# Optimization experiments

Measured on AMD Instinct MI355X. Metric: run time of the kernel, lower is better.

The kernel has to match this reference:

```python
import jax, jax.numpy as jnp
import numpy as np

K = 4          # deform conv kernel size
STRIDE = 4     # deform conv stride (no padding)
EPS = 1e-5     # BatchNorm eps
SLOPE = 0.01   # LeakyReLU default negative slope


def conv2d(x, w, b, stride):
    out = jax.lax.conv_general_dilated(
        x, w, (stride, stride), 'VALID',
        dimension_numbers=('NCHW', 'OIHW', 'NCHW'))
    return out + b[None, :, None, None]


def batchnorm(x, g, b, m, v):
    inv = g / jnp.sqrt(v + EPS)
    return x * inv[None, :, None, None] + (b - m * inv)[None, :, None, None]


def leaky_relu(x):
    return jnp.where(x >= 0, x, SLOPE * x)


def deform_conv(x, offset, w, b):
    # x: [B,C,H,W], offset: [B,2*K*K,Ho,Wo] with (dy,dx) interleaved per kernel tap
    B, C, H, W = x.shape
    Ho, Wo = offset.shape[2], offset.shape[3]
    KK = K * K
    off = offset.reshape(B, KK, 2, Ho, Wo)
    kh = jnp.repeat(jnp.arange(K), K).astype(x.dtype)   # [KK] kernel row
    kw = jnp.tile(jnp.arange(K), K).astype(x.dtype)     # [KK] kernel col
    base_y = (jnp.arange(Ho) * STRIDE).astype(x.dtype)
    base_x = (jnp.arange(Wo) * STRIDE).astype(x.dtype)
    # sampling coordinates [B,KK,Ho,Wo]
    py = base_y[None, None, :, None] + kh[None, :, None, None] + off[:, :, 0]
    px = base_x[None, None, None, :] + kw[None, :, None, None] + off[:, :, 1]
    y0 = jnp.floor(py)
    x0 = jnp.floor(px)
    wy = py - y0
    wx = px - x0

    def corner(yc, xc):
        yi = yc.astype(jnp.int32)
        xi = xc.astype(jnp.int32)
        valid = (yi >= 0) & (yi < H) & (xi >= 0) & (xi < W)
        yi = jnp.clip(yi, 0, H - 1)
        xi = jnp.clip(xi, 0, W - 1)
        # per-batch gather: [B,C,KK,Ho,Wo]
        v = jax.vmap(lambda img, a, c: img[:, a, c])(x, yi, xi)
        return v * valid[:, None].astype(x.dtype)

    v00 = corner(y0, x0)
    v01 = corner(y0, x0 + 1)
    v10 = corner(y0 + 1, x0)
    v11 = corner(y0 + 1, x0 + 1)
    wy_ = wy[:, None]
    wx_ = wx[:, None]
    sampled = (v00 * (1 - wy_) * (1 - wx_) + v01 * (1 - wy_) * wx_
               + v10 * wy_ * (1 - wx_) + v11 * wy_ * wx_)  # [B,C,KK,Ho,Wo]
    out = jnp.einsum('bckhw,ock->bohw', sampled, w.reshape(w.shape[0], C, KK))
    return out + b[None, :, None, None]


def setup_inputs() -> dict:
    key = jax.random.key(0)
    ks = jax.random.split(key, 16)
    f32 = jnp.float32
    inp = {
        'x': jax.random.normal(ks[0], (64, 3, 224, 224), f32),
        'stem_w': jax.random.normal(ks[1], (96, 3, 4, 4), f32) * 0.1,
        'stem_b': jax.random.normal(ks[2], (96,), f32) * 0.05,
        'bn1_g': jax.random.uniform(ks[3], (96,), f32, 0.5, 1.5),
        'bn1_b': jax.random.normal(ks[4], (96,), f32) * 0.05,
        'bn1_m': jax.random.normal(ks[5], (96,), f32) * 0.05,
        'bn1_v': jax.random.uniform(ks[6], (96,), f32, 0.5, 1.5),
        'off_w': jax.random.normal(ks[7], (32, 96, 4, 4), f32) * 0.02,
        'off_b': jax.random.normal(ks[8], (32,), f32) * 0.02,
        'dcn_w': jax.random.normal(ks[9], (768, 96, 4, 4), f32) * 0.05,
        'dcn_b': jax.random.normal(ks[10], (768,), f32) * 0.05,
        'bn2_g': jax.random.uniform(ks[11], (768,), f32, 0.5, 1.5),
        'bn2_b': jax.random.normal(ks[12], (768,), f32) * 0.05,
        'bn2_m': jax.random.normal(ks[13], (768,), f32) * 0.05,
        'bn2_v': jax.random.uniform(ks[14], (768,), f32, 0.5, 1.5),
    }
    return inp


def reference(x, stem_w, stem_b, bn1_g, bn1_b, bn1_m, bn1_v,
              off_w, off_b, dcn_w, dcn_b, bn2_g, bn2_b, bn2_m, bn2_v):
    h = conv2d(x, stem_w, stem_b, 4)                      # [B,96,56,56]
    h = leaky_relu(batchnorm(h, bn1_g, bn1_b, bn1_m, bn1_v))
    offset = conv2d(h, off_w, off_b, 4)                   # [B,32,14,14]
    h = deform_conv(h, offset, dcn_w, dcn_b)              # [B,768,14,14]
    h = leaky_relu(batchnorm(h, bn2_g, bn2_b, bn2_m, bn2_v))
    B, C, Ho, Wo = h.shape
    return h.reshape(B, C, Ho * Wo).transpose(0, 2, 1)    # [B,196,768]
```

## Files before the change

### kernel.cpp

```cpp
#include <hip/hip_runtime.h>

#define EPS   1e-5f
#define SLOPE 0.01f

#define WS_H1B  0L
#define WS_OFF  9633792L
#define WS_S1   10035200L
#define WS_T1   10035296L
#define WS_T2   10035392L
#define WS_SB   10036160L
#define WS_WTB  19669952L
#define WS_WOB  20259776L
#define WS_W1B  20284352L

__device__ __forceinline__ unsigned short f2bf(float f) {
    unsigned int u = __builtin_bit_cast(unsigned int, f);
    u += 0x7fffu + ((u >> 16) & 1u);
    return (unsigned short)(u >> 16);
}
__device__ __forceinline__ float bf2f(unsigned short u) {
    unsigned int t = ((unsigned int)u) << 16;
    return __builtin_bit_cast(float, t);
}

typedef __attribute__((ext_vector_type(4))) unsigned short ushort4v;
typedef __attribute__((ext_vector_type(8))) unsigned short ushort8v;
typedef __attribute__((ext_vector_type(8))) short bf16x8;
typedef __attribute__((ext_vector_type(4))) float floatx4;

__global__ __launch_bounds__(256) void k0_prep(
    const float* __restrict__ stem_w, const float* __restrict__ stem_b,
    const float* __restrict__ bn1_g,  const float* __restrict__ bn1_b,
    const float* __restrict__ bn1_m,  const float* __restrict__ bn1_v,
    const float* __restrict__ off_w,  const float* __restrict__ dcn_w,
    const float* __restrict__ dcn_b,  const float* __restrict__ bn2_g,
    const float* __restrict__ bn2_b,  const float* __restrict__ bn2_m,
    const float* __restrict__ bn2_v,  float* __restrict__ ws)
{
    const int tid = threadIdx.x;
    const int blk = blockIdx.x;
    unsigned short* Wtb = (unsigned short*)(ws + WS_WTB);
    unsigned short* Wob = (unsigned short*)(ws + WS_WOB);
    unsigned short* W1b = (unsigned short*)(ws + WS_W1B);

    if (blk < 800) {
        __shared__ float row[1536];
        const int oc = (blk < 768) ? blk : blk - 768;
        const float* src = (blk < 768) ? (dcn_w + (long)oc * 1536)
                                       : (off_w + (long)oc * 1536);
        for (int i = tid; i < 1536; i += 256) row[i] = src[i];
        float sc = 1.f;
        if (blk < 768) sc = bn2_g[oc] * rsqrtf(bn2_v[oc] + EPS);
        __syncthreads();
        if (tid < 192) {
            int k0 = tid * 8;
            ushort8v o;
#pragma unroll
            for (int t = 0; t < 8; t++) {
                int k = k0 + t;
                int kk = k / 96, c = k % 96;
                ((unsigned short*)&o)[t] = f2bf(row[c * 16 + kk] * sc);
            }
            unsigned short* dst = (blk < 768) ? (Wtb + (long)oc * 1536 + k0)
                                              : (Wob + (long)oc * 1536 + k0);
            *(ushort8v*)dst = o;
        }
    } else {
        for (int i = tid; i < 6144; i += 256) {
            int ks = i / 3072, rr = i % 3072;
            int oc = rr >> 5, kl = rr & 31;
            int k = ks * 32 + kl;
            W1b[i] = f2bf(k < 48 ? stem_w[oc * 48 + k] : 0.f);
        }
        if (tid < 96) {
            float s = bn1_g[tid] * rsqrtf(bn1_v[tid] + EPS);
            ws[WS_S1 + tid] = s;
            ws[WS_T1 + tid] = stem_b[tid] * s + bn1_b[tid] - bn1_m[tid] * s;
        }
        for (int i = tid; i < 768; i += 256) {
            float inv2 = bn2_g[i] * rsqrtf(bn2_v[i] + EPS);
            ws[WS_T2 + i] = dcn_b[i] * inv2 + bn2_b[i] - bn2_m[i] * inv2;
        }
    }
}

__global__ __launch_bounds__(256) void k1_stem_mfma(
    const float* __restrict__ x, const unsigned short* __restrict__ W1b,
    const float* __restrict__ s1, const float* __restrict__ t1,
    unsigned short* __restrict__ h1)
{
    const int tid  = threadIdx.x;
    const int wave = tid >> 6, lane = tid & 63;
    const int m = lane & 15, quad = lane >> 4;
    const int p0 = blockIdx.x * 128;

    __shared__ unsigned short sm[14336];
    unsigned short* sA = sm;
    unsigned short* sB = sm + 8192;

#pragma unroll
    for (int i = 0; i < 3; i++) {
        int inst = wave * 3 + i;
        const unsigned short* g = W1b + inst * 512 + lane * 8;
        __builtin_amdgcn_global_load_lds(
            (const __attribute__((address_space(1))) void*)g,
            (__attribute__((address_space(3))) void*)(sB + inst * 512), 16, 0, 0);
    }

    {
        int r = tid >> 1, off = 16 + (tid & 1) * 8;
        *(ushort8v*)&sA[4096 + r * 32 + off] = (ushort8v)0;
    }

#pragma unroll
    for (int i = 0; i < 6; i++) {
        int unit = i * 256 + tid;
        int r = unit & 127, s = unit >> 7;
        int ci = s >> 2, kh = s & 3;
        int p = p0 + r;
        int b = p / 3136, rem = p % 3136;
        int oy = rem / 56, ox = rem % 56;
        float4 v = *(const float4*)&x[((long)((b * 3 + ci) * 224 + oy * 4 + kh)) * 224 + ox * 4];
        ushort4v hv;
        hv.x = f2bf(v.x); hv.y = f2bf(v.y); hv.z = f2bf(v.z); hv.w = f2bf(v.w);
        int k0i = ci * 16 + kh * 4;
        *(ushort4v*)&sA[(k0i >> 5) * 4096 + r * 32 + (k0i & 31)] = hv;
    }
    __syncthreads();

    bf16x8 bfv[6][2], af[2][2];
#pragma unroll
    for (int j = 0; j < 6; j++)
#pragma unroll
        for (int ks = 0; ks < 2; ks++)
            bfv[j][ks] = *(const bf16x8*)&sB[ks * 3072 + (j * 16 + m) * 32 + quad * 8];
#pragma unroll
    for (int rt = 0; rt < 2; rt++)
#pragma unroll
        for (int ks = 0; ks < 2; ks++)
            af[rt][ks] = *(const bf16x8*)&sA[ks * 4096 + (wave * 32 + rt * 16 + m) * 32 + quad * 8];

    floatx4 acc[2][6];
#pragma unroll
    for (int rt = 0; rt < 2; rt++)
#pragma unroll
        for (int j = 0; j < 6; j++) {
            floatx4 a = (floatx4)0.f;
            a = __builtin_amdgcn_mfma_f32_16x16x32_bf16(af[rt][0], bfv[j][0], a, 0, 0, 0);
            a = __builtin_amdgcn_mfma_f32_16x16x32_bf16(af[rt][1], bfv[j][1], a, 0, 0, 0);
            acc[rt][j] = a;
        }

    __syncthreads();
#pragma unroll
    for (int j = 0; j < 6; j++) {
        int c = j * 16 + m;
        float sc = s1[c], bi = t1[c];
#pragma unroll
        for (int rt = 0; rt < 2; rt++)
#pragma unroll
            for (int r = 0; r < 4; r++) {
                int row = wave * 32 + rt * 16 + quad * 4 + r;
                float v = acc[rt][j][r] * sc + bi;
                v = v >= 0.f ? v : SLOPE * v;
                sm[row * 96 + c] = f2bf(v);
            }
    }
    __syncthreads();
#pragma unroll
    for (int i = 0; i < 6; i++) {
        int idx = (i * 256 + tid) * 8;
        *(ushort8v*)&h1[(long)p0 * 96 + idx] = *(const ushort8v*)&sm[idx];
    }
}

__global__ __launch_bounds__(256) void k2_mfma(
    const unsigned short* __restrict__ h1,
    const unsigned short* __restrict__ Wob,
    const float* __restrict__ off_b, float* __restrict__ off)
{
    const int tid  = threadIdx.x;
    const int wave = tid >> 6;
    const int lane = tid & 63;
    const int n0   = blockIdx.x * 128;
    const int m    = lane & 15;
    const int quad = lane >> 4;

    __shared__ unsigned short sA[128 * 32];
    __shared__ unsigned short sB[32 * 32];

    const int skoff = (lane & 3) * 8;
    int n_a = n0 + wave * 32 + (lane >> 2);
    int n_b = n_a + 16;
    int ba = n_a / 196, pa = n_a % 196;
    int bb = n_b / 196, pb = n_b % 196;
    long pixa = ((long)(ba * 56 + (pa / 14) * 4) * 56 + (pa % 14) * 4);
    long pixb = ((long)(bb * 56 + (pb / 14) * 4) * 56 + (pb % 14) * 4);

    const unsigned short* gB = Wob + (long)((wave & 1) * 16 + (lane >> 2)) * 1536 + skoff;
    unsigned short* lA0 = &sA[(wave * 32 +  0) * 32];
    unsigned short* lA1 = &sA[(wave * 32 + 16) * 32];
    unsigned short* lB  = &sB[((wave & 1) * 16) * 32];

    floatx4 acc[2][2];
#pragma unroll
    for (int i = 0; i < 2; i++)
#pragma unroll
        for (int j = 0; j < 2; j++) acc[i][j] = (floatx4)0.f;

    for (int kt = 0; kt < 48; ++kt) {
        int khw = kt / 3;
        int c0  = (kt - khw * 3) * 32;
        int kh  = khw >> 2, kw = khw & 3;
        long eoff = (long)(kh * 56 + kw) * 96 + c0 + skoff;
        const unsigned short* gA0 = h1 + pixa * 96 + eoff;
        const unsigned short* gA1 = h1 + pixb * 96 + eoff;

        __syncthreads();
        __builtin_amdgcn_global_load_lds(
            (const __attribute__((address_space(1))) void*)gA0,
            (__attribute__((address_space(3))) void*)lA0, 16, 0, 0);
        __builtin_amdgcn_global_load_lds(
            (const __attribute__((address_space(1))) void*)gA1,
            (__attribute__((address_space(3))) void*)lA1, 16, 0, 0);
        if (wave < 2)
            __builtin_amdgcn_global_load_lds(
                (const __attribute__((address_space(1))) void*)gB,
                (__attribute__((address_space(3))) void*)lB, 16, 0, 0);
        gB += 32;
        __syncthreads();

        bf16x8 af[2], bfr[2];
#pragma unroll
        for (int i = 0; i < 2; i++)
            af[i] = *(const bf16x8*)&sA[(wave * 32 + i * 16 + m) * 32 + quad * 8];
#pragma unroll
        for (int j = 0; j < 2; j++)
            bfr[j] = *(const bf16x8*)&sB[(j * 16 + m) * 32 + quad * 8];
#pragma unroll
        for (int i = 0; i < 2; i++)
#pragma unroll
            for (int j = 0; j < 2; j++)
                acc[i][j] = __builtin_amdgcn_mfma_f32_16x16x32_bf16(
                    af[i], bfr[j], acc[i][j], 0, 0, 0);
    }

    float tb[2];
#pragma unroll
    for (int j = 0; j < 2; j++) tb[j] = off_b[j * 16 + m];
#pragma unroll
    for (int i = 0; i < 2; i++)
#pragma unroll
        for (int r = 0; r < 4; r++) {
            long n = n0 + wave * 32 + i * 16 + quad * 4 + r;
#pragma unroll
            for (int j = 0; j < 2; j++)
                off[n * 32 + j * 16 + m] = acc[i][j][r] + tb[j];
        }
}

__global__ __launch_bounds__(384) void k3_sample(
    const unsigned short* __restrict__ h1, const float* __restrict__ off,
    unsigned short* __restrict__ S)
{
    const int p = blockIdx.x;
    const int b = blockIdx.y;
    const int y = p / 14, xo = p % 14;
    const int tid = threadIdx.x;
    const int c4 = tid % 24, kk = tid / 24;
    const int kh = kk >> 2, kw = kk & 3;

    const float* ob = off + ((long)(b * 196 + p)) * 32;
    float dy = ob[kk * 2];
    float dx = ob[kk * 2 + 1];

    float py = (float)(y * 4 + kh) + dy;
    float px = (float)(xo * 4 + kw) + dx;
    float y0f = floorf(py), x0f = floorf(px);
    float wy = py - y0f, wx = px - x0f;
    int y0 = (int)y0f, x0 = (int)x0f;
    int y1 = y0 + 1,  x1 = x0 + 1;

    float my0 = (y0 >= 0 && y0 < 56) ? 1.f : 0.f;
    float my1 = (y1 >= 0 && y1 < 56) ? 1.f : 0.f;
    float mx0 = (x0 >= 0 && x0 < 56) ? 1.f : 0.f;
    float mx1 = (x1 >= 0 && x1 < 56) ? 1.f : 0.f;
    int y0c = min(max(y0, 0), 55), y1c = min(max(y1, 0), 55);
    int x0c = min(max(x0, 0), 55), x1c = min(max(x1, 0), 55);

    const unsigned short* hb = h1 + (long)b * 56 * 56 * 96 + c4 * 4;
    ushort4v v00 = *(const ushort4v*)&hb[(y0c * 56 + x0c) * 96];
    ushort4v v01 = *(const ushort4v*)&hb[(y0c * 56 + x1c) * 96];
    ushort4v v10 = *(const ushort4v*)&hb[(y1c * 56 + x0c) * 96];
    ushort4v v11 = *(const ushort4v*)&hb[(y1c * 56 + x1c) * 96];

    float w00 = my0 * mx0 * (1.f - wy) * (1.f - wx);
    float w01 = my0 * mx1 * (1.f - wy) * wx;
    float w10 = my1 * mx0 * wy * (1.f - wx);
    float w11 = my1 * mx1 * wy * wx;

    ushort4v rr;
#pragma unroll
    for (int c = 0; c < 4; c++) {
        float v = bf2f(((unsigned short*)&v00)[c]) * w00
                + bf2f(((unsigned short*)&v01)[c]) * w01
                + bf2f(((unsigned short*)&v10)[c]) * w10
                + bf2f(((unsigned short*)&v11)[c]) * w11;
        ((unsigned short*)&rr)[c] = f2bf(v);
    }

    long n = (long)b * 196 + p;
    *(ushort4v*)&S[n * 1536 + kk * 96 + c4 * 4] = rr;
}

__global__ __launch_bounds__(256) void k4_gemm_mfma(
    const unsigned short* __restrict__ S,
    const unsigned short* __restrict__ Wtb,
    const float* __restrict__ t2, float* __restrict__ out)
{
    const int tid  = threadIdx.x;
    const int wave = tid >> 6;
    const int lane = tid & 63;

    int lid = blockIdx.x + blockIdx.y * 6;
    int xcd = lid & 7, s = lid >> 3;
    int work = (xcd < 4) ? (xcd * 74 + s) : (296 + (xcd - 4) * 73 + s);
    const int oc0 = (work % 6) * 128;
    const int n0  = (work / 6) * 128;

    const int wr  = wave >> 1, wc = wave & 1;
    const int m    = lane & 15;
    const int quad = lane >> 4;

    __shared__ unsigned short sA[2][128 * 32];
    __shared__ unsigned short sB[2][128 * 32];

    const int srow  = wave * 32 + (lane >> 2);
    const int skoff = (lane & 3) * 8;
    const unsigned short* gA0 = S   + (long)(n0  + srow) * 1536 + skoff;
    const unsigned short* gA1 = gA0 + 16L * 1536;
    const unsigned short* gB0 = Wtb + (long)(oc0 + srow) * 1536 + skoff;
    const unsigned short* gB1 = gB0 + 16L * 1536;
    unsigned short* lA0 = &sA[0][(wave * 32 +  0) * 32];
    unsigned short* lA1 = &sA[0][(wave * 32 + 16) * 32];
    unsigned short* lB0 = &sB[0][(wave * 32 +  0) * 32];
    unsigned short* lB1 = &sB[0][(wave * 32 + 16) * 32];
    const int bufstride = 128 * 32;

    floatx4 acc[4][4];
#pragma unroll
    for (int i = 0; i < 4; i++)
#pragma unroll
        for (int j = 0; j < 4; j++) acc[i][j] = (floatx4)0.f;

    for (int kt = 0; kt < 24; ++kt) {
        __syncthreads();
        __builtin_amdgcn_global_load_lds(
            (const __attribute__((address_space(1))) void*)gA0,
            (__attribute__((address_space(3))) void*)lA0, 16, 0, 0);
        __builtin_amdgcn_global_load_lds(
            (const __attribute__((address_space(1))) void*)gA1,
            (__attribute__((address_space(3))) void*)lA1, 16, 0, 0);
        __builtin_amdgcn_global_load_lds(
            (const __attribute__((address_space(1))) void*)gB0,
            (__attribute__((address_space(3))) void*)lB0, 16, 0, 0);
        __builtin_amdgcn_global_load_lds(
            (const __attribute__((address_space(1))) void*)gB1,
            (__attribute__((address_space(3))) void*)lB1, 16, 0, 0);
        __builtin_amdgcn_global_load_lds(
            (const __attribute__((address_space(1))) void*)(gA0 + 32),
            (__attribute__((address_space(3))) void*)(lA0 + bufstride), 16, 0, 0);
        __builtin_amdgcn_global_load_lds(
            (const __attribute__((address_space(1))) void*)(gA1 + 32),
            (__attribute__((address_space(3))) void*)(lA1 + bufstride), 16, 0, 0);
        __builtin_amdgcn_global_load_lds(
            (const __attribute__((address_space(1))) void*)(gB0 + 32),
            (__attribute__((address_space(3))) void*)(lB0 + bufstride), 16, 0, 0);
        __builtin_amdgcn_global_load_lds(
            (const __attribute__((address_space(1))) void*)(gB1 + 32),
            (__attribute__((address_space(3))) void*)(lB1 + bufstride), 16, 0, 0);
        gA0 += 64; gA1 += 64; gB0 += 64; gB1 += 64;
        __syncthreads();

#pragma unroll
        for (int h = 0; h < 2; h++) {
            bf16x8 af[4], bf[4];
#pragma unroll
            for (int i = 0; i < 4; i++)
                af[i] = *(const bf16x8*)&sA[h][(wr * 64 + i * 16 + m) * 32 + quad * 8];
#pragma unroll
            for (int j = 0; j < 4; j++)
                bf[j] = *(const bf16x8*)&sB[h][(wc * 64 + j * 16 + m) * 32 + quad * 8];
#pragma unroll
            for (int i = 0; i < 4; i++)
#pragma unroll
                for (int j = 0; j < 4; j++)
                    acc[i][j] = __builtin_amdgcn_mfma_f32_16x16x32_bf16(
                        af[i], bf[j], acc[i][j], 0, 0, 0);
        }
    }

    float tb[4];
#pragma unroll
    for (int j = 0; j < 4; j++) tb[j] = t2[oc0 + wc * 64 + j * 16 + m];
#pragma unroll
    for (int i = 0; i < 4; i++) {
#pragma unroll
        for (int r = 0; r < 4; r++) {
            long n = n0 + wr * 64 + i * 16 + quad * 4 + r;
            float* orow = out + n * 768 + oc0 + wc * 64 + m;
#pragma unroll
            for (int j = 0; j < 4; j++) {
                float v = acc[i][j][r] + tb[j];
                orow[j * 16] = v >= 0.f ? v : SLOPE * v;
            }
        }
    }
}

extern "C" void kernel_launch(void* const* d_in, const int* in_sizes, int n_in,
                              void* d_out, int out_size, void* d_ws, size_t ws_size,
                              hipStream_t stream)
{
    const float* x      = (const float*)d_in[0];
    const float* stem_w = (const float*)d_in[1];
    const float* stem_b = (const float*)d_in[2];
    const float* bn1_g  = (const float*)d_in[3];
    const float* bn1_b  = (const float*)d_in[4];
    const float* bn1_m  = (const float*)d_in[5];
    const float* bn1_v  = (const float*)d_in[6];
    const float* off_w  = (const float*)d_in[7];
    const float* off_b  = (const float*)d_in[8];
    const float* dcn_w  = (const float*)d_in[9];
    const float* dcn_b  = (const float*)d_in[10];
    const float* bn2_g  = (const float*)d_in[11];
    const float* bn2_b  = (const float*)d_in[12];
    const float* bn2_m  = (const float*)d_in[13];
    const float* bn2_v  = (const float*)d_in[14];

    float* ws  = (float*)d_ws;
    float* out = (float*)d_out;

    unsigned short* h1  = (unsigned short*)(ws + WS_H1B);
    float* off = ws + WS_OFF;
    float* s1  = ws + WS_S1;
    float* t1  = ws + WS_T1;
    float* t2  = ws + WS_T2;
    unsigned short* Sb  = (unsigned short*)(ws + WS_SB);
    unsigned short* Wtb = (unsigned short*)(ws + WS_WTB);
    unsigned short* Wob = (unsigned short*)(ws + WS_WOB);
    unsigned short* W1b = (unsigned short*)(ws + WS_W1B);

    k0_prep<<<801, 256, 0, stream>>>(stem_w, stem_b, bn1_g, bn1_b, bn1_m, bn1_v,
                                     off_w, dcn_w, dcn_b, bn2_g, bn2_b, bn2_m,
                                     bn2_v, ws);
    k1_stem_mfma<<<1568, 256, 0, stream>>>(x, W1b, s1, t1, h1);
    k2_mfma<<<98, 256, 0, stream>>>(h1, Wob, off_b, off);
    k3_sample<<<dim3(196, 64), 384, 0, stream>>>(h1, off, Sb);
    k4_gemm_mfma<<<dim3(6, 98), 256, 0, stream>>>(Sb, Wtb, t2, out);
}
```

Before: 224.2 us.

## Split-K the offset conv GEMM and shrink DCN GEMM tiles for more blocks

The offset conv kernel is split four ways along K across 392 blocks, with an atomic-add epilogue onto a zeroed buffer and the bias added only by the first split. Its loads are now double-buffered so the next tile is fetched while the current one is computed. The main DCN GEMM moves from 128x128 tiles to 128x64 tiles, giving 1176 blocks instead of 588, with single-tile double buffering and a new XCD-aware block remap. This is meant to fill the GPU better on two undersized grids, at the cost of atomics, an extra memset, and less data reuse per block in the big GEMM.

```diff
diff --git a/kernel.cpp b/kernel.cpp
--- a/kernel.cpp
+++ b/kernel.cpp
@@ -106,12 +106,10 @@
             (const __attribute__((address_space(1))) void*)g,
             (__attribute__((address_space(3))) void*)(sB + inst * 512), 16, 0, 0);
     }
-
     {
         int r = tid >> 1, off = 16 + (tid & 1) * 8;
         *(ushort8v*)&sA[4096 + r * 32 + off] = (ushort8v)0;
     }
-
 #pragma unroll
     for (int i = 0; i < 6; i++) {
         int unit = i * 256 + tid;
@@ -180,14 +178,13 @@
     const float* __restrict__ off_b, float* __restrict__ off)
 {
     const int tid  = threadIdx.x;
-    const int wave = tid >> 6;
-    const int lane = tid & 63;
-    const int n0   = blockIdx.x * 128;
-    const int m    = lane & 15;
-    const int quad = lane >> 4;
-
-    __shared__ unsigned short sA[128 * 32];
-    __shared__ unsigned short sB[32 * 32];
+    const int wave = tid >> 6, lane = tid & 63;
+    const int m = lane & 15, quad = lane >> 4;
+    const int nt = blockIdx.x % 98, ks = blockIdx.x / 98;
+    const int n0 = nt * 128;
+
+    __shared__ unsigned short sA[2][4096];
+    __shared__ unsigned short sB[2][1024];
 
     const int skoff = (lane & 3) * 8;
     int n_a = n0 + wave * 32 + (lane >> 2);
@@ -197,46 +194,47 @@
     long pixa = ((long)(ba * 56 + (pa / 14) * 4) * 56 + (pa % 14) * 4);
     long pixb = ((long)(bb * 56 + (pb / 14) * 4) * 56 + (pb % 14) * 4);
 
-    const unsigned short* gB = Wob + (long)((wave & 1) * 16 + (lane >> 2)) * 1536 + skoff;
-    unsigned short* lA0 = &sA[(wave * 32 +  0) * 32];
-    unsigned short* lA1 = &sA[(wave * 32 + 16) * 32];
-    unsigned short* lB  = &sB[((wave & 1) * 16) * 32];
-
-    floatx4 acc[2][2];
-#pragma unroll
-    for (int i = 0; i < 2; i++)
-#pragma unroll
-        for (int j = 0; j < 2; j++) acc[i][j] = (floatx4)0.f;
-
-    for (int kt = 0; kt < 48; ++kt) {
-        int khw = kt / 3;
-        int c0  = (kt - khw * 3) * 32;
+    const unsigned short* gB = Wob + (long)(wave * 16 + (lane >> 2)) * 1536 + ks * 384 + skoff;
+    const int lofA0 = (wave * 32) * 32;
+    const int lofA1 = (wave * 32 + 16) * 32;
+    const int lofB  = (wave * 16) * 32;
+
+    auto issue = [&](int buf, int kt) {
+        int khw = ks * 4 + kt / 3;
+        int c0  = (kt % 3) * 32;
         int kh  = khw >> 2, kw = khw & 3;
         long eoff = (long)(kh * 56 + kw) * 96 + c0 + skoff;
-        const unsigned short* gA0 = h1 + pixa * 96 + eoff;
-        const unsigned short* gA1 = h1 + pixb * 96 + eoff;
-
-        __syncthreads();
-        __builtin_amdgcn_global_load_lds(
-            (const __attribute__((address_space(1))) void*)gA0,
-            (__attribute__((address_space(3))) void*)lA0, 16, 0, 0);
-        __builtin_amdgcn_global_load_lds(
-            (const __attribute__((address_space(1))) void*)gA1,
-            (__attribute__((address_space(3))) void*)lA1, 16, 0, 0);
+        __builtin_amdgcn_global_load_lds(
+            (const __attribute__((address_space(1))) void*)(h1 + pixa * 96 + eoff),
+            (__attribute__((address_space(3))) void*)&sA[buf][lofA0], 16, 0, 0);
+        __builtin_amdgcn_global_load_lds(
+            (const __attribute__((address_space(1))) void*)(h1 + pixb * 96 + eoff),
+            (__attribute__((address_space(3))) void*)&sA[buf][lofA1], 16, 0, 0);
         if (wave < 2)
             __builtin_amdgcn_global_load_lds(
-                (const __attribute__((address_space(1))) void*)gB,
-                (__attribute__((address_space(3))) void*)lB, 16, 0, 0);
-        gB += 32;
+                (const __attribute__((address_space(1))) void*)(gB + kt * 32),
+                (__attribute__((address_space(3))) void*)&sB[buf][lofB], 16, 0, 0);
+    };
+
+    floatx4 acc[2][2];
+#pragma unroll
+    for (int i = 0; i < 2; i++)
+#pragma unroll
+        for (int j = 0; j < 2; j++) acc[i][j] = (floatx4)0.f;
+
+    issue(0, 0);
+    for (int kt = 0; kt < 12; ++kt) {
         __syncthreads();
-
+        if (kt < 11) issue((kt + 1) & 1, kt + 1);
+        const unsigned short* bufA = sA[kt & 1];
+        const unsigned short* bufB = sB[kt & 1];
         bf16x8 af[2], bfr[2];
 #pragma unroll
         for (int i = 0; i < 2; i++)
-            af[i] = *(const bf16x8*)&sA[(wave * 32 + i * 16 + m) * 32 + quad * 8];
+            af[i] = *(const bf16x8*)&bufA[(wave * 32 + i * 16 + m) * 32 + quad * 8];
 #pragma unroll
         for (int j = 0; j < 2; j++)
-            bfr[j] = *(const bf16x8*)&sB[(j * 16 + m) * 32 + quad * 8];
+            bfr[j] = *(const bf16x8*)&bufB[(j * 16 + m) * 32 + quad * 8];
 #pragma unroll
         for (int i = 0; i < 2; i++)
 #pragma unroll
@@ -247,7 +245,7 @@
 
     float tb[2];
 #pragma unroll
-    for (int j = 0; j < 2; j++) tb[j] = off_b[j * 16 + m];
+    for (int j = 0; j < 2; j++) tb[j] = (ks == 0) ? off_b[j * 16 + m] : 0.f;
 #pragma unroll
     for (int i = 0; i < 2; i++)
 #pragma unroll
@@ -255,7 +253,7 @@
             long n = n0 + wave * 32 + i * 16 + quad * 4 + r;
 #pragma unroll
             for (int j = 0; j < 2; j++)
-                off[n * 32 + j * 16 + m] = acc[i][j][r] + tb[j];
+                atomicAdd(&off[n * 32 + j * 16 + m], acc[i][j][r] + tb[j]);
         }
 }
 
@@ -319,98 +317,78 @@
     const float* __restrict__ t2, float* __restrict__ out)
 {
     const int tid  = threadIdx.x;
-    const int wave = tid >> 6;
-    const int lane = tid & 63;
-
-    int lid = blockIdx.x + blockIdx.y * 6;
-    int xcd = lid & 7, s = lid >> 3;
-    int work = (xcd < 4) ? (xcd * 74 + s) : (296 + (xcd - 4) * 73 + s);
-    const int oc0 = (work % 6) * 128;
-    const int n0  = (work / 6) * 128;
-
-    const int wr  = wave >> 1, wc = wave & 1;
-    const int m    = lane & 15;
-    const int quad = lane >> 4;
-
-    __shared__ unsigned short sA[2][128 * 32];
-    __shared__ unsigned short sB[2][128 * 32];
-
-    const int srow  = wave * 32 + (lane >> 2);
+    const int wave = tid >> 6, lane = tid & 63;
+
+    int lid = blockIdx.x;
+    int work = (lid & 7) * 147 + (lid >> 3);
+    const int n0  = (work / 12) * 128;
+    const int oc0 = (work % 12) * 64;
+
+    const int wr = wave >> 1, wc = wave & 1;
+    const int m = lane & 15, quad = lane >> 4;
+
+    __shared__ unsigned short sA[2][4096];
+    __shared__ unsigned short sB[2][2048];
+
     const int skoff = (lane & 3) * 8;
-    const unsigned short* gA0 = S   + (long)(n0  + srow) * 1536 + skoff;
+    const unsigned short* gA0 = S + (long)(n0 + wave * 32 + (lane >> 2)) * 1536 + skoff;
     const unsigned short* gA1 = gA0 + 16L * 1536;
-    const unsigned short* gB0 = Wtb + (long)(oc0 + srow) * 1536 + skoff;
-    const unsigned short* gB1 = gB0 + 16L * 1536;
-    unsigned short* lA0 = &sA[0][(wave * 32 +  0) * 32];
-    unsigned short* lA1 = &sA[0][(wave * 32 + 16) * 32];
-    unsigned short* lB0 = &sB[0][(wave * 32 +  0) * 32];
-    unsigned short* lB1 = &sB[0][(wave * 32 + 16) * 32];
-    const int bufstride = 128 * 32;
-
-    floatx4 acc[4][4];
+    const unsigned short* gB  = Wtb + (long)(oc0 + wave * 16 + (lane >> 2)) * 1536 + skoff;
+    const int lofA0 = (wave * 32) * 32;
+    const int lofA1 = (wave * 32 + 16) * 32;
+    const int lofB  = (wave * 16) * 32;
+
+    auto issue = [&](int buf) {
+        __builtin_amdgcn_global_load_lds(
+            (const __attribute__((address_space(1))) void*)gA0,
+            (__attribute__((address_space(3))) void*)&sA[buf][lofA0], 16, 0, 0);
+        __builtin_amdgcn_global_load_lds(
+            (const __attribute__((address_space(1))) void*)gA1,
+            (__attribute__((address_space(3))) void*)&sA[buf][lofA1], 16, 0, 0);
+        __builtin_amdgcn_global_load_lds(
+            (const __attribute__((address_space(1))) void*)gB,
+            (__attribute__((address_space(3))) void*)&sB[buf][lofB], 16, 0, 0);
+        gA0 += 32; gA1 += 32; gB += 32;
+    };
+
+    floatx4 acc[4][2];
 #pragma unroll
     for (int i = 0; i < 4; i++)
 #pragma unroll
-        for (int j = 0; j < 4; j++) acc[i][j] = (floatx4)0.f;
-
-    for (int kt = 0; kt < 24; ++kt) {
+        for (int j = 0; j < 2; j++) acc[i][j] = (floatx4)0.f;
+
+    issue(0);
+    for (int kt = 0; kt < 48; ++kt) {
         __syncthreads();
-        __builtin_amdgcn_global_load_lds(
-            (const __attribute__((address_space(1))) void*)gA0,
-            (__attribute__((address_space(3))) void*)lA0, 16, 0, 0);
-        __builtin_amdgcn_global_load_lds(
-            (const __attribute__((address_space(1))) void*)gA1,
-            (__attribute__((address_space(3))) void*)lA1, 16, 0, 0);
-        __builtin_amdgcn_global_load_lds(
-            (const __attribute__((address_space(1))) void*)gB0,
-            (__attribute__((address_space(3))) void*)lB0, 16, 0, 0);
-        __builtin_amdgcn_global_load_lds(
-            (const __attribute__((address_space(1))) void*)gB1,
-            (__attribute__((address_space(3))) void*)lB1, 16, 0, 0);
-        __builtin_amdgcn_global_load_lds(
-            (const __attribute__((address_space(1))) void*)(gA0 + 32),
-            (__attribute__((address_space(3))) void*)(lA0 + bufstride), 16, 0, 0);
-        __builtin_amdgcn_global_load_lds(
-            (const __attribute__((address_space(1))) void*)(gA1 + 32),
-            (__attribute__((address_space(3))) void*)(lA1 + bufstride), 16, 0, 0);
-        __builtin_amdgcn_global_load_lds(
-            (const __attribute__((address_space(1))) void*)(gB0 + 32),
-            (__attribute__((address_space(3))) void*)(lB0 + bufstride), 16, 0, 0);
-        __builtin_amdgcn_global_load_lds(
-            (const __attribute__((address_space(1))) void*)(gB1 + 32),
-            (__attribute__((address_space(3))) void*)(lB1 + bufstride), 16, 0, 0);
-        gA0 += 64; gA1 += 64; gB0 += 64; gB1 += 64;
-        __syncthreads();
-
-#pragma unroll
-        for (int h = 0; h < 2; h++) {
-            bf16x8 af[4], bf[4];
-#pragma unroll
-            for (int i = 0; i < 4; i++)
-                af[i] = *(const bf16x8*)&sA[h][(wr * 64 + i * 16 + m) * 32 + quad * 8];
-#pragma unroll
-            for (int j = 0; j < 4; j++)
-                bf[j] = *(const bf16x8*)&sB[h][(wc * 64 + j * 16 + m) * 32 + quad * 8];
-#pragma unroll
-            for (int i = 0; i < 4; i++)
-#pragma unroll
-                for (int j = 0; j < 4; j++)
-                    acc[i][j] = __builtin_amdgcn_mfma_f32_16x16x32_bf16(
-                        af[i], bf[j], acc[i][j], 0, 0, 0);
-        }
-    }
-
-    float tb[4];
-#pragma unroll
-    for (int j = 0; j < 4; j++) tb[j] = t2[oc0 + wc * 64 + j * 16 + m];
+        if (kt < 47) issue((kt + 1) & 1);
+        const unsigned short* bufA = sA[kt & 1];
+        const unsigned short* bufB = sB[kt & 1];
+        bf16x8 af[4], bf[2];
+#pragma unroll
+        for (int i = 0; i < 4; i++)
+            af[i] = *(const bf16x8*)&bufA[(wr * 64 + i * 16 + m) * 32 + quad * 8];
+#pragma unroll
+        for (int j = 0; j < 2; j++)
+            bf[j] = *(const bf16x8*)&bufB[(wc * 32 + j * 16 + m) * 32 + quad * 8];
+#pragma unroll
+        for (int i = 0; i < 4; i++)
+#pragma unroll
+            for (int j = 0; j < 2; j++)
+                acc[i][j] = __builtin_amdgcn_mfma_f32_16x16x32_bf16(
+                    af[i], bf[j], acc[i][j], 0, 0, 0);
+    }
+
+    float tb[2];
+#pragma unroll
+    for (int j = 0; j < 2; j++) tb[j] = t2[oc0 + wc * 32 + j * 16 + m];
 #pragma unroll
     for (int i = 0; i < 4; i++) {
 #pragma unroll
         for (int r = 0; r < 4; r++) {
             long n = n0 + wr * 64 + i * 16 + quad * 4 + r;
-            float* orow = out + n * 768 + oc0 + wc * 64 + m;
-#pragma unroll
-            for (int j = 0; j < 4; j++) {
+            float* orow = out + n * 768 + oc0 + wc * 32 + m;
+#pragma unroll
+            for (int j = 0; j < 2; j++) {
                 float v = acc[i][j][r] + tb[j];
                 orow[j * 16] = v >= 0.f ? v : SLOPE * v;
             }
@@ -454,8 +432,9 @@
     k0_prep<<<801, 256, 0, stream>>>(stem_w, stem_b, bn1_g, bn1_b, bn1_m, bn1_v,
                                      off_w, dcn_w, dcn_b, bn2_g, bn2_b, bn2_m,
                                      bn2_v, ws);
+    hipMemsetAsync(off, 0, 401408 * sizeof(float), stream);
     k1_stem_mfma<<<1568, 256, 0, stream>>>(x, W1b, s1, t1, h1);
-    k2_mfma<<<98, 256, 0, stream>>>(h1, Wob, off_b, off);
+    k2_mfma<<<392, 256, 0, stream>>>(h1, Wob, off_b, off);
     k3_sample<<<dim3(196, 64), 384, 0, stream>>>(h1, off, Sb);
-    k4_gemm_mfma<<<dim3(6, 98), 256, 0, stream>>>(Sb, Wtb, t2, out);
-}
+    k4_gemm_mfma<<<1176, 256, 0, stream>>>(Sb, Wtb, t2, out);
+}
```

Result: faster. 216.5 us (-3.5%).
